# Optimization experiments

Measured on AMD Instinct MI355X. Metric: run time of the kernel, lower is better.

The kernel has to match this reference:

```python
import jax, jax.numpy as jnp
import numpy as np

B, S, D, N, LAYERS = 512, 64, 256, 100000, 1


def setup_inputs() -> dict:
    key = jax.random.key(0)
    ks = jax.random.split(key, 9)
    stdv = 1.0 / np.sqrt(D)
    return {
        "embedding": jax.random.uniform(ks[0], (N, D), jnp.float32, -stdv, stdv),
        "W1": jax.random.uniform(ks[1], (2 * D, 2 * D), jnp.float32, -stdv, stdv),
        "W2": jax.random.uniform(ks[2], (2 * D, D), jnp.float32, -stdv, stdv),
        "adj_in": jax.random.uniform(ks[3], (B, S, S), jnp.float32),
        "adj_out": jax.random.uniform(ks[4], (B, S, S), jnp.float32),
        "mask": jnp.ones((B, S), jnp.float32),
        "item": jax.random.randint(ks[5], (B, S), 0, N),
        "alias": jax.random.randint(ks[6], (B, S), 0, S),
        "tar": jax.random.randint(ks[7], (B,), 1, N),  # targets in [1, n_node)
    }


def reference(embedding, W1, W2, adj_in, adj_out, mask, item, alias, tar):
    # ---- sgc(): gather -> dual adjacency aggregation -> concat -> 2-layer MLP
    fin = embedding[item]                              # [B,S,D]
    # torch `adj ** layers` is elementwise power (not matrix power)
    fs_in = jnp.matmul(adj_in ** LAYERS, fin)          # [B,S,D]
    fs_out = jnp.matmul(adj_out ** LAYERS, fin)        # [B,S,D]
    av = jnp.concatenate([fs_in, fs_out], axis=-1)     # [B,S,2D]
    av = jnp.matmul(jax.nn.relu(jnp.matmul(av, W1)), W2)  # [B,S,D]

    # ---- forward(): pick last node's hidden, score against item table
    rows = jnp.arange(B)
    rm = jnp.sum(mask, axis=1).astype(jnp.int32)       # session lengths [B]
    last_id = alias[rows, rm - 1]                      # [B]
    last_h = av[rows, last_id]                         # [B,D]
    logits = last_h @ embedding[1:].T                  # [B,N-1]

    logp = jax.nn.log_softmax(logits, axis=-1)
    loss = -jnp.mean(logp[rows, tar - 1])
    # L2 term is zero: params live in a plain dict (not registered) and l2=0.
    return loss, logits
```

## Files before the change

kernel.cpp:

```cpp
#include <hip/hip_runtime.h>
#include <cstdint>
#include <cstddef>

#define BDIM 512
#define SDIM 64
#define DDIM 256
#define D2   512
#define NNODE 100000
#define NM1  99999

typedef short short8 __attribute__((ext_vector_type(8)));
typedef float f32x4 __attribute__((ext_vector_type(4)));

__device__ __forceinline__ unsigned short f2bf(float f) {
  unsigned int u = __float_as_uint(f);
  u += 0x7FFFu + ((u >> 16) & 1u);
  return (unsigned short)(u >> 16);
}

__global__ __launch_bounds__(256) void prep_kernel(
    const float* __restrict__ emb, const float* __restrict__ adj_in,
    const float* __restrict__ adj_out, const float* __restrict__ mask,
    const int* __restrict__ item, const int* __restrict__ alias_,
    float* __restrict__ av) {
  __shared__ float a_in[SDIM], a_out[SDIM];
  __shared__ int it[SDIM];
  __shared__ int s_star;
  const int b = blockIdx.x, t = threadIdx.x;
  if (t < SDIM) it[t] = item[b * SDIM + t];
  if (t < 64) {
    float m = mask[b * SDIM + t];
#pragma unroll
    for (int off = 32; off > 0; off >>= 1) m += __shfl_down(m, off, 64);
    if (t == 0) {
      int rm = (int)m;
      s_star = alias_[b * SDIM + rm - 1];
    }
  }
  __syncthreads();
  const int ss = s_star;
  if (t < SDIM) a_in[t] = adj_in[((size_t)b * SDIM + ss) * SDIM + t];
  else if (t < 2 * SDIM) a_out[t - SDIM] = adj_out[((size_t)b * SDIM + ss) * SDIM + (t - SDIM)];
  __syncthreads();
  const int d = t;
  float ai = 0.f, ao = 0.f;
#pragma unroll 8
  for (int j = 0; j < SDIM; j++) {
    float e = emb[(size_t)it[j] * DDIM + d];
    ai = fmaf(a_in[j], e, ai);
    ao = fmaf(a_out[j], e, ao);
  }
  av[(size_t)b * D2 + d] = ai;
  av[(size_t)b * D2 + DDIM + d] = ao;
}

template <int N, bool RELU, bool OUTBF16>
__global__ __launch_bounds__(256) void mlp_kernel(
    const float* __restrict__ A, const float* __restrict__ W,
    float* __restrict__ Of, unsigned short* __restrict__ Ob) {
  __shared__ float As[32][36];
  __shared__ float Bs[32][68];
  const int tx = threadIdx.x, ty = threadIdx.y;
  const int t = ty * 16 + tx;
  const int row0 = blockIdx.y * 32, col0 = blockIdx.x * 64;
  const int ar = t >> 3, ac = (t & 7) * 4;
  const int kr = t >> 4, bc = (t & 15) * 4;
  float acc[2][4];
#pragma unroll
  for (int i = 0; i < 2; i++)
#pragma unroll
    for (int j = 0; j < 4; j++) acc[i][j] = 0.f;

  for (int k0 = 0; k0 < D2; k0 += 32) {
    const float4 a4 = *(const float4*)&A[(size_t)(row0 + ar) * D2 + k0 + ac];
    const float4 b4a = *(const float4*)&W[(size_t)(k0 + kr) * N + col0 + bc];
    const float4 b4b = *(const float4*)&W[(size_t)(k0 + kr + 16) * N + col0 + bc];
    *(float4*)&As[ar][ac] = a4;
    *(float4*)&Bs[kr][bc] = b4a;
    *(float4*)&Bs[kr + 16][bc] = b4b;
    __syncthreads();
#pragma unroll
    for (int k = 0; k < 32; k++) {
      const float a0 = As[ty * 2][k];
      const float a1 = As[ty * 2 + 1][k];
      const float4 bv = *(const float4*)&Bs[k][tx * 4];
      acc[0][0] = fmaf(a0, bv.x, acc[0][0]); acc[0][1] = fmaf(a0, bv.y, acc[0][1]);
      acc[0][2] = fmaf(a0, bv.z, acc[0][2]); acc[0][3] = fmaf(a0, bv.w, acc[0][3]);
      acc[1][0] = fmaf(a1, bv.x, acc[1][0]); acc[1][1] = fmaf(a1, bv.y, acc[1][1]);
      acc[1][2] = fmaf(a1, bv.z, acc[1][2]); acc[1][3] = fmaf(a1, bv.w, acc[1][3]);
    }
    __syncthreads();
  }
#pragma unroll
  for (int i = 0; i < 2; i++) {
    const int row = row0 + ty * 2 + i;
    const int col = col0 + tx * 4;
    float4 r4;
    r4.x = acc[i][0]; r4.y = acc[i][1]; r4.z = acc[i][2]; r4.w = acc[i][3];
    if constexpr (RELU) {
      r4.x = fmaxf(r4.x, 0.f); r4.y = fmaxf(r4.y, 0.f);
      r4.z = fmaxf(r4.z, 0.f); r4.w = fmaxf(r4.w, 0.f);
    }
    if constexpr (OUTBF16) {
      ushort4 p;
      p.x = f2bf(r4.x); p.y = f2bf(r4.y); p.z = f2bf(r4.z); p.w = f2bf(r4.w);
      *(ushort4*)&Ob[(size_t)row * N + col] = p;
    } else {
      *(float4*)&Of[(size_t)row * N + col] = r4;
    }
  }
}

#define NT    64
#define BPAD  264
#define NCHUNK 391

__global__ __launch_bounds__(512, 4) void logits_gemm(
    const unsigned short* __restrict__ Abf,
    const float* __restrict__ emb,
    float* __restrict__ out,
    float* __restrict__ part) {
  __shared__ short Bs[NT * BPAD];
  __shared__ float rse_s[256];
  const int t = threadIdx.x;
  const int lane = t & 63, w = t >> 6;
  const int nchunk = blockIdx.x;
  const int mbase = blockIdx.y * 256;
  const int wm = w * 32;
  const int c = lane & 15, q = lane >> 4;

  float s8[8];
#pragma unroll
  for (int i = 0; i < 8; i++) s8[i] = 0.f;

#pragma unroll 1
  for (int st = 0; st < 4; st++) {
    const int nbase = nchunk * 256 + st * NT;

    __syncthreads();
    {
      const int row = t >> 3;
      const int cb = (t & 7) * 4;
      int er = nbase + row + 1;
      if (er > NM1) er = NM1;
      const float* src = emb + (size_t)er * DDIM;
      short* dst = &Bs[row * BPAD];
#pragma unroll
      for (int j = 0; j < 8; j++) {
        const float4 v = *(const float4*)(src + j * 32 + cb);
        ushort4 p;
        p.x = f2bf(v.x); p.y = f2bf(v.y); p.z = f2bf(v.z); p.w = f2bf(v.w);
        *(ushort4*)&dst[j * 32 + cb] = p;
      }
    }
    __syncthreads();

    f32x4 acc[2][4];
#pragma unroll
    for (int mi = 0; mi < 2; mi++)
#pragma unroll
      for (int ni = 0; ni < 4; ni++) acc[mi][ni] = (f32x4){0.f, 0.f, 0.f, 0.f};

#pragma unroll
    for (int ks = 0; ks < 8; ks++) {
      short8 afr[2], bfr[4];
#pragma unroll
      for (int mi = 0; mi < 2; mi++)
        afr[mi] = *(const short8*)(Abf +
            (size_t)(mbase + wm + mi * 16 + c) * DDIM + ks * 32 + q * 8);
#pragma unroll
      for (int ni = 0; ni < 4; ni++)
        bfr[ni] = *(const short8*)&Bs[(ni * 16 + c) * BPAD + ks * 32 + q * 8];
#pragma unroll
      for (int mi = 0; mi < 2; mi++)
#pragma unroll
        for (int ni = 0; ni < 4; ni++)
          acc[mi][ni] = __builtin_amdgcn_mfma_f32_16x16x32_bf16(
              afr[mi], bfr[ni], acc[mi][ni], 0, 0, 0);
    }

    const bool full = (nbase + NT <= NM1);
#pragma unroll
    for (int mi = 0; mi < 2; mi++) {
#pragma unroll
      for (int r = 0; r < 4; r++) {
        const int grow = mbase + wm + mi * 16 + q * 4 + r;
        float s = 0.f;
        if (full) {
#pragma unroll
          for (int ni = 0; ni < 4; ni++) {
            const float v = acc[mi][ni][r];
            out[1 + (size_t)grow * NM1 + nbase + ni * 16 + c] = v;
            s += __expf(v);
          }
        } else {
#pragma unroll
          for (int ni = 0; ni < 4; ni++) {
            const int col = nbase + ni * 16 + c;
            if (col < NM1) {
              const float v = acc[mi][ni][r];
              out[1 + (size_t)grow * NM1 + col] = v;
              s += __expf(v);
            }
          }
        }
        s8[mi * 4 + r] += s;
      }
    }
  }

#pragma unroll
  for (int mi = 0; mi < 2; mi++) {
#pragma unroll
    for (int r = 0; r < 4; r++) {
      float s = s8[mi * 4 + r];
#pragma unroll
      for (int msk = 1; msk < 16; msk <<= 1) s += __shfl_xor(s, msk, 64);
      if (c == 0) rse_s[wm + mi * 16 + q * 4 + r] = s;
    }
  }
  __syncthreads();
  if (t < 256) part[(size_t)nchunk * BDIM + mbase + t] = rse_s[t];
}

__global__ __launch_bounds__(256) void rse_loss_kernel(
    const float* __restrict__ part, const float* __restrict__ out,
    const int* __restrict__ tar, float* __restrict__ lossv) {
  const int b = blockIdx.x;
  const int t = threadIdx.x;
  float s = 0.f;
  for (int j = t; j < NCHUNK; j += 256)
    s += part[(size_t)j * BDIM + b];
  __shared__ float red[4];
#pragma unroll
  for (int off = 32; off > 0; off >>= 1) s += __shfl_down(s, off, 64);
  if ((t & 63) == 0) red[t >> 6] = s;
  __syncthreads();
  if (t == 0) {
    const float tot = red[0] + red[1] + red[2] + red[3];
    const int tt = tar[b];
    const float lg = out[1 + (size_t)b * NM1 + (tt - 1)];
    lossv[b] = logf(tot) - lg;
  }
}

__global__ __launch_bounds__(512) void loss_final_kernel(
    float* __restrict__ out, const float* __restrict__ lossv) {
  __shared__ float red[512];
  const int t = threadIdx.x;
  red[t] = lossv[t];
  __syncthreads();
  for (int stride = 256; stride > 0; stride >>= 1) {
    if (t < stride) red[t] += red[t + stride];
    __syncthreads();
  }
  if (t == 0) out[0] = red[0] / (float)BDIM;
}

extern "C" void kernel_launch(void* const* d_in, const int* in_sizes, int n_in,
                              void* d_out, int out_size, void* d_ws, size_t ws_size,
                              hipStream_t stream) {
  const float* emb     = (const float*)d_in[0];
  const float* W1      = (const float*)d_in[1];
  const float* W2      = (const float*)d_in[2];
  const float* adj_in  = (const float*)d_in[3];
  const float* adj_out = (const float*)d_in[4];
  const float* mask    = (const float*)d_in[5];
  const int*   item    = (const int*)d_in[6];
  const int*   alias_  = (const int*)d_in[7];
  const int*   tar     = (const int*)d_in[8];
  float* out = (float*)d_out;

  char* ws = (char*)d_ws;
  float* av            = (float*)(ws);
  float* h1            = (float*)(ws + 1048576);
  unsigned short* lasth = (unsigned short*)(ws + 2097152);
  float* part          = (float*)(ws + 2359296);
  float* lossv         = (float*)(ws + 5560320);

  prep_kernel<<<BDIM, 256, 0, stream>>>(emb, adj_in, adj_out, mask, item, alias_, av);
  mlp_kernel<D2, true, false><<<dim3(8, 16), dim3(16, 16), 0, stream>>>(av, W1, h1, nullptr);
  mlp_kernel<DDIM, false, true><<<dim3(4, 16), dim3(16, 16), 0, stream>>>(h1, W2, nullptr, lasth);
  logits_gemm<<<dim3(NCHUNK, 2), 512, 0, stream>>>(lasth, emb, out, part);
  rse_loss_kernel<<<BDIM, 256, 0, stream>>>(part, out, tar, lossv);
  loss_final_kernel<<<1, 512, 0, stream>>>(out, lossv);
}
```

Before: 463.1 us.

## Retile logits GEMM to 128-row blocks and batch the output writes

Each logits_gemm block now covers 128 batch rows instead of 256, and the grid becomes 4 x 391, with the M blocks ordered fastest so the blocks sharing one embedding chunk are adjacent. Each wave keeps accumulators for all four 64-column sub-tiles and writes its full 256-column strip at the end, which gives longer contiguous stores per row. The aim is better write coalescing and more blocks for scheduling. In exchange, each embedding chunk is converted to bf16 four times instead of twice, and the 64 accumulator registers per lane may reduce occupancy.

Result: faster. 448.8 us (-3.1%).

```diff
diff --git a/kernel.cpp b/kernel.cpp
--- a/kernel.cpp
+++ b/kernel.cpp
@@ -121,19 +121,21 @@
     float* __restrict__ out,
     float* __restrict__ part) {
   __shared__ short Bs[NT * BPAD];
-  __shared__ float rse_s[256];
+  __shared__ float rse_s[128];
   const int t = threadIdx.x;
   const int lane = t & 63, w = t >> 6;
-  const int nchunk = blockIdx.x;
-  const int mbase = blockIdx.y * 256;
-  const int wm = w * 32;
+  const int mbase = blockIdx.x * 128;
+  const int nchunk = blockIdx.y;
   const int c = lane & 15, q = lane >> 4;
-
-  float s8[8];
-#pragma unroll
-  for (int i = 0; i < 8; i++) s8[i] = 0.f;
-
-#pragma unroll 1
+  const int wrow = w * 16;
+
+  f32x4 acc[4][4];
+#pragma unroll
+  for (int st = 0; st < 4; st++)
+#pragma unroll
+    for (int ni = 0; ni < 4; ni++) acc[st][ni] = (f32x4){0.f, 0.f, 0.f, 0.f};
+
+#pragma unroll
   for (int st = 0; st < 4; st++) {
     const int nbase = nchunk * 256 + st * NT;
 
@@ -155,72 +157,73 @@
     }
     __syncthreads();
 
-    f32x4 acc[2][4];
-#pragma unroll
-    for (int mi = 0; mi < 2; mi++)
-#pragma unroll
-      for (int ni = 0; ni < 4; ni++) acc[mi][ni] = (f32x4){0.f, 0.f, 0.f, 0.f};
-
 #pragma unroll
     for (int ks = 0; ks < 8; ks++) {
-      short8 afr[2], bfr[4];
-#pragma unroll
-      for (int mi = 0; mi < 2; mi++)
-        afr[mi] = *(const short8*)(Abf +
-            (size_t)(mbase + wm + mi * 16 + c) * DDIM + ks * 32 + q * 8);
+      const short8 afr = *(const short8*)(Abf +
+          (size_t)(mbase + wrow + c) * DDIM + ks * 32 + q * 8);
+      short8 bfr[4];
 #pragma unroll
       for (int ni = 0; ni < 4; ni++)
         bfr[ni] = *(const short8*)&Bs[(ni * 16 + c) * BPAD + ks * 32 + q * 8];
 #pragma unroll
-      for (int mi = 0; mi < 2; mi++)
-#pragma unroll
-        for (int ni = 0; ni < 4; ni++)
-          acc[mi][ni] = __builtin_amdgcn_mfma_f32_16x16x32_bf16(
-              afr[mi], bfr[ni], acc[mi][ni], 0, 0, 0);
-    }
-
-    const bool full = (nbase + NT <= NM1);
-#pragma unroll
-    for (int mi = 0; mi < 2; mi++) {
-#pragma unroll
-      for (int r = 0; r < 4; r++) {
-        const int grow = mbase + wm + mi * 16 + q * 4 + r;
-        float s = 0.f;
-        if (full) {
-#pragma unroll
-          for (int ni = 0; ni < 4; ni++) {
-            const float v = acc[mi][ni][r];
-            out[1 + (size_t)grow * NM1 + nbase + ni * 16 + c] = v;
+      for (int ni = 0; ni < 4; ni++)
+        acc[st][ni] = __builtin_amdgcn_mfma_f32_16x16x32_bf16(
+            afr, bfr[ni], acc[st][ni], 0, 0, 0);
+    }
+  }
+
+  float s4[4];
+#pragma unroll
+  for (int r = 0; r < 4; r++) s4[r] = 0.f;
+
+  const int cbase = nchunk * 256;
+  if (cbase + 256 <= NM1) {
+#pragma unroll
+    for (int r = 0; r < 4; r++) {
+      const int grow = mbase + wrow + q * 4 + r;
+      float* orow = out + 1 + (size_t)grow * NM1 + cbase + c;
+      float s = 0.f;
+#pragma unroll
+      for (int st = 0; st < 4; st++) {
+#pragma unroll
+        for (int ni = 0; ni < 4; ni++) {
+          const float v = acc[st][ni][r];
+          orow[st * 64 + ni * 16] = v;
+          s += __expf(v);
+        }
+      }
+      s4[r] = s;
+    }
+  } else {
+#pragma unroll
+    for (int r = 0; r < 4; r++) {
+      const int grow = mbase + wrow + q * 4 + r;
+      float s = 0.f;
+#pragma unroll
+      for (int st = 0; st < 4; st++) {
+#pragma unroll
+        for (int ni = 0; ni < 4; ni++) {
+          const int col = cbase + st * 64 + ni * 16 + c;
+          if (col < NM1) {
+            const float v = acc[st][ni][r];
+            out[1 + (size_t)grow * NM1 + col] = v;
             s += __expf(v);
           }
-        } else {
-#pragma unroll
-          for (int ni = 0; ni < 4; ni++) {
-            const int col = nbase + ni * 16 + c;
-            if (col < NM1) {
-              const float v = acc[mi][ni][r];
-              out[1 + (size_t)grow * NM1 + col] = v;
-              s += __expf(v);
-            }
-          }
         }
-        s8[mi * 4 + r] += s;
       }
-    }
-  }
-
-#pragma unroll
-  for (int mi = 0; mi < 2; mi++) {
-#pragma unroll
-    for (int r = 0; r < 4; r++) {
-      float s = s8[mi * 4 + r];
-#pragma unroll
-      for (int msk = 1; msk < 16; msk <<= 1) s += __shfl_xor(s, msk, 64);
-      if (c == 0) rse_s[wm + mi * 16 + q * 4 + r] = s;
-    }
-  }
-  __syncthreads();
-  if (t < 256) part[(size_t)nchunk * BDIM + mbase + t] = rse_s[t];
+      s4[r] = s;
+    }
+  }
+
+#pragma unroll
+  for (int r = 0; r < 4; r++) {
+    float s = s4[r];
+#pragma unroll
+    for (int msk = 1; msk < 16; msk <<= 1) s += __shfl_xor(s, msk, 64);
+    if (c == 0) rse_s[wrow + q * 4 + r] = s;
+  }
+  __syncthreads();
+  if (t < 128) part[(size_t)nchunk * BDIM + mbase + t] = rse_s[t];
 }
 
 __global__ __launch_bounds__(256) void rse_loss_kernel(
@@ -281,7 +284,7 @@
   prep_kernel<<<BDIM, 256, 0, stream>>>(emb, adj_in, adj_out, mask, item, alias_, av);
   mlp_kernel<D2, true, false><<<dim3(8, 16), dim3(16, 16), 0, stream>>>(av, W1, h1, nullptr);
   mlp_kernel<DDIM, false, true><<<dim3(4, 16), dim3(16, 16), 0, stream>>>(h1, W2, nullptr, lasth);
-  logits_gemm<<<dim3(NCHUNK, 2), 512, 0, stream>>>(lasth, emb, out, part);
+  logits_gemm<<<dim3(4, NCHUNK), 512, 0, stream>>>(lasth, emb, out, part);
   rse_loss_kernel<<<BDIM, 256, 0, stream>>>(part, out, tar, lossv);
   loss_final_kernel<<<1, 512, 0, stream>>>(out, lossv);
 }
```
